# Kernel optimization log

Measured on AMD Instinct MI355X. Metric: run time of the kernel, lower is better.

Reference implementation:

```python
import jax, jax.numpy as jnp
import numpy as np

HEAD_SIZE = 64


def setup_inputs() -> dict:
    key = jax.random.key(0)
    k1, k2, k3, k4 = jax.random.split(key, 4)
    B, T, E = 8, 2048, 1024
    x = jax.random.normal(k1, (B, T, E), dtype=jnp.float32)
    # nn.Linear(n_embd, head_size, bias=False) weights: [head_size, n_embd]
    s = 1.0 / np.sqrt(E)
    Wk = jax.random.uniform(k2, (HEAD_SIZE, E), jnp.float32, -s, s)
    Wq = jax.random.uniform(k3, (HEAD_SIZE, E), jnp.float32, -s, s)
    Wv = jax.random.uniform(k4, (HEAD_SIZE, E), jnp.float32, -s, s)
    return {"x": x, "Wk": Wk, "Wq": Wq, "Wv": Wv}


def reference(x, Wk, Wq, Wv):
    # x: [B, T, E]; W*: [D, E] with D = head_size
    B, T, E = x.shape
    k = jnp.einsum("bte,de->btd", x, Wk)  # [B,T,D]
    q = jnp.einsum("bte,de->btd", x, Wq)
    v = jnp.einsum("bte,de->btd", x, Wv)
    scale = k.shape[-1] ** -0.5
    wei = jnp.einsum("btd,bsd->bts", q, k) * scale  # [B,T,T]
    causal = jnp.tril(jnp.ones((T, T), dtype=bool))
    wei = jnp.where(causal, wei, -jnp.inf)
    wei = jax.nn.softmax(wei, axis=-1)
    # dropout p=0.0 (eval): identity
    return jnp.einsum("bts,bsd->btd", wei, v)
```

## Files before the change

### kernel.cpp

```cpp
#include <hip/hip_runtime.h>
#include <hip/hip_bf16.h>


typedef __bf16 bf16x8 __attribute__((ext_vector_type(8)));
typedef float  f32x4  __attribute__((ext_vector_type(4)));

#define T_SEQ 2048
#define E_DIM 1024
#define D_HEAD 64
#define M_TOT 16384
#define NSPLIT 4
#define SC_LOG2E 0.18033688011112042f

__device__ __forceinline__ unsigned short f2b(float f) {
  union { float f; unsigned int u; } cv; cv.f = f;
  unsigned int u = cv.u;
  u += 0x7FFFu + ((u >> 16) & 1u);
  return (unsigned short)(u >> 16);
}

__device__ __forceinline__ unsigned int f2b2(float a, float b) {
#if __has_builtin(__builtin_amdgcn_cvt_pk_bf16_f32)
  typedef __bf16 bf16x2_t __attribute__((ext_vector_type(2)));
  union { bf16x2_t v; unsigned int u; } cv;
  cv.v = __builtin_amdgcn_cvt_pk_bf16_f32(a, b);
  return cv.u;
#else
  return (unsigned int)f2b(a) | ((unsigned int)f2b(b) << 16);
#endif
}

__global__ __launch_bounds__(256) void wcvt_kernel(
    const float* __restrict__ Wk, const float* __restrict__ Wq,
    const float* __restrict__ Wv, unsigned short* __restrict__ WbF)
{
  int i = blockIdx.x * 256 + threadIdx.x;
  int n = i >> 8, c4 = i & 255;
  const float* src = (n < 64) ? Wq + n * E_DIM
                   : (n < 128) ? Wk + (n - 64) * E_DIM
                               : Wv + (n - 128) * E_DIM;
  float4 v = *(const float4*)(src + c4 * 4);
  int k = c4 * 4, kb = k >> 5, kk = k & 31;
  *(uint2*)(WbF + (size_t)(kb * 192 + n) * 32 + kk) =
      make_uint2(f2b2(v.x, v.y), f2b2(v.z, v.w));
}

__global__ __launch_bounds__(256, 4) void proj_kernel(
    const float* __restrict__ x, const unsigned short* __restrict__ WbF,
    unsigned short* __restrict__ qws, unsigned short* __restrict__ kfws,
    unsigned short* __restrict__ vfws)
{
  __shared__ __align__(16) unsigned short x_lds[16 * 1024];

  const int tid = threadIdx.x, wv = tid >> 6, lane = tid & 63;
  const int c = lane & 15, quad = lane >> 4;
  const int m0 = blockIdx.x * 16;
  const int b = m0 >> 11, tloc = m0 & 2047;

  for (int j = 0; j < 16; ++j) {
    float4 v = *(const float4*)(x + (size_t)(m0 + j) * E_DIM + tid * 4);
    int chunk = tid >> 1, half = tid & 1;
    int phys = chunk ^ (j & 7);
    *(uint2*)&x_lds[j * 1024 + phys * 8 + half * 4] =
        make_uint2(f2b2(v.x, v.y), f2b2(v.z, v.w));
  }
  __syncthreads();

  f32x4 acc[3];
  for (int j = 0; j < 3; ++j)
    for (int r = 0; r < 4; ++r) acc[j][r] = 0.0f;

  const unsigned short* bbase[3];
  for (int j = 0; j < 3; ++j)
    bbase[j] = WbF + (size_t)((wv * 3 + j) * 16 + c) * 32 + quad * 8;

  bf16x8 bcur[3], bnxt[3];
  for (int j = 0; j < 3; ++j) bcur[j] = *(const bf16x8*)(bbase[j]);

  for (int kb = 0; kb < 32; ++kb) {
    if (kb < 31)
      for (int j = 0; j < 3; ++j)
        bnxt[j] = *(const bf16x8*)(bbase[j] + (size_t)(kb + 1) * 6144);
    bf16x8 a = *(const bf16x8*)&x_lds[c * 1024 + (((kb * 4 + quad) ^ (c & 7)) << 3)];
    for (int j = 0; j < 3; ++j)
      acc[j] = __builtin_amdgcn_mfma_f32_16x16x32_bf16(a, bcur[j], acc[j], 0, 0, 0);
    for (int j = 0; j < 3; ++j) bcur[j] = bnxt[j];
  }

  const int rloc = tloc + quad * 4;
  for (int j = 0; j < 3; ++j) {
    const int nt = wv * 3 + j;
    if (nt < 4) {
      int d = nt * 16 + c;
      for (int r = 0; r < 4; ++r)
        qws[(size_t)(m0 + quad * 4 + r) * D_HEAD + d] = f2b(acc[j][r] * SC_LOG2E);
    } else if (nt < 8) {
      int d = (nt - 4) * 16 + c;
      size_t base = ((size_t)(b * 2 + (d >> 5)) * T_SEQ + rloc) * 32 + (d & 31);
      for (int r = 0; r < 4; ++r)
        kfws[base + (size_t)r * 32] = f2b(acc[j][r]);
    } else {
      int d = (nt - 8) * 16 + c;
      size_t base = ((size_t)(b * 64 + (rloc >> 5)) * 64 + d) * 32 + (rloc & 31);
      *(ushort4*)&vfws[base] =
          make_ushort4(f2b(acc[j][0]), f2b(acc[j][1]), f2b(acc[j][2]), f2b(acc[j][3]));
    }
  }
}

__global__ __launch_bounds__(256, 4) void attn_kernel(
    const unsigned short* __restrict__ qws, const unsigned short* __restrict__ kfws,
    const unsigned short* __restrict__ vfws,
    unsigned short* __restrict__ opart, float* __restrict__ lpart)
{
  __shared__ __align__(16) unsigned short p_lds[64 * 64];

  const int tid = threadIdx.x, wv = tid >> 6, lane = tid & 63;
  const int c = lane & 15, quad = lane >> 4;
  const int qt = blockIdx.x, b = blockIdx.y, sg = blockIdx.z;
  const int t0 = qt * 64;
  const size_t qkb = (size_t)b * T_SEQ * D_HEAD;
  const int niter = (qt >= sg) ? ((qt - sg) >> 2) + 1 : 0;
  const int rloc = wv * 16 + quad * 4;
  const size_t prow = ((size_t)sg * 8 + b) * T_SEQ;

  if (niter == 0) {
    for (int nt = 0; nt < 4; ++nt)
      for (int r = 0; r < 4; ++r)
        opart[(prow + t0 + rloc + r) * D_HEAD + nt * 16 + c] = 0;
    if (c == 0)
      for (int r = 0; r < 4; ++r) lpart[prow + t0 + rloc + r] = 0.0f;
    return;
  }

  const int mrow = wv * 16 + c;
  const bf16x8 qf0 = *(const bf16x8*)(qws + qkb + (size_t)(t0 + mrow) * D_HEAD + quad * 8);
  const bf16x8 qf1 = *(const bf16x8*)(qws + qkb + (size_t)(t0 + mrow) * D_HEAD + 32 + quad * 8);

  bf16x8 ones;
  { union { unsigned short s[8]; bf16x8 v; } o;
    for (int i = 0; i < 8; ++i) o.s[i] = 0x3F80;
    ones = o.v; }

  f32x4 acc_o[4], acc_l;
  for (int r = 0; r < 4; ++r) acc_l[r] = 0.0f;
  for (int nt = 0; nt < 4; ++nt)
    for (int r = 0; r < 4; ++r) acc_o[nt][r] = 0.0f;

  const unsigned short* Kb = kfws + (size_t)b * 2 * T_SEQ * 32;
  const unsigned short* Vb = vfws + (size_t)b * 64 * D_HEAD * 32;
  const bool mydiag = (sg == (qt & 3));

  for (int it = 0; it < niter; ++it) {
    const int s0 = (sg + 4 * it) * 64;

    bf16x8 kf[8];
    for (int nt = 0; nt < 4; ++nt)
      for (int kb = 0; kb < 2; ++kb)
        kf[nt * 2 + kb] = *(const bf16x8*)(Kb + ((size_t)kb * T_SEQ + s0 + nt * 16 + c) * 32 + quad * 8);

    bf16x8 vf[8];
    for (int ks = 0; ks < 2; ++ks) {
      int sb = (s0 >> 5) + ks;
      for (int nt = 0; nt < 4; ++nt)
        vf[ks * 4 + nt] = *(const bf16x8*)(Vb + ((size_t)sb * 64 + nt * 16 + c) * 32 + quad * 8);
    }

    f32x4 accs[4];
    for (int nt = 0; nt < 4; ++nt)
      for (int r = 0; r < 4; ++r) accs[nt][r] = 0.0f;
    for (int nt = 0; nt < 4; ++nt) {
      accs[nt] = __builtin_amdgcn_mfma_f32_16x16x32_bf16(qf0, kf[nt * 2], accs[nt], 0, 0, 0);
      accs[nt] = __builtin_amdgcn_mfma_f32_16x16x32_bf16(qf1, kf[nt * 2 + 1], accs[nt], 0, 0, 0);
    }
    if (mydiag && it == niter - 1) {
      for (int nt = 0; nt < 4; ++nt) {
        int scol = s0 + nt * 16 + c;
        for (int r = 0; r < 4; ++r)
          if (scol > t0 + rloc + r) accs[nt][r] = -__builtin_inff();
      }
    }

    for (int nt = 0; nt < 4; ++nt)
      for (int r = 0; r < 4; ++r)
        accs[nt][r] = __builtin_exp2f(accs[nt][r]);

    for (int nt = 0; nt < 4; ++nt)
      for (int r = 0; r < 4; ++r) {
        int rr = rloc + r;
        p_lds[rr * 64 + (((nt * 2 + (c >> 3)) ^ (rr & 7)) << 3) + (c & 7)] = f2b(accs[nt][r]);
      }

    for (int ks = 0; ks < 2; ++ks) {
      int kg = ks * 4 + quad;
      bf16x8 pf = *(const bf16x8*)&p_lds[mrow * 64 + ((kg ^ (mrow & 7)) << 3)];
      acc_l = __builtin_amdgcn_mfma_f32_16x16x32_bf16(pf, ones, acc_l, 0, 0, 0);
      for (int nt = 0; nt < 4; ++nt)
        acc_o[nt] = __builtin_amdgcn_mfma_f32_16x16x32_bf16(pf, vf[ks * 4 + nt], acc_o[nt], 0, 0, 0);
    }
  }

  for (int nt = 0; nt < 4; ++nt)
    for (int r = 0; r < 4; ++r)
      opart[(prow + t0 + rloc + r) * D_HEAD + nt * 16 + c] = f2b(acc_o[nt][r]);
  if (c == 0)
    for (int r = 0; r < 4; ++r) lpart[prow + t0 + rloc + r] = acc_l[r];
}

__global__ __launch_bounds__(256) void merge_kernel(
    const unsigned short* __restrict__ opart, const float* __restrict__ lpart,
    float* __restrict__ out)
{
  int gid = blockIdx.x * 256 + threadIdx.x;
  int gr = gid >> 4, d4 = (gid & 15) * 4;
  float L = 0.0f;
  for (int i = 0; i < NSPLIT; ++i) L += lpart[(size_t)i * M_TOT + gr];
  float inv = 1.0f / L;
  float4 o = make_float4(0.f, 0.f, 0.f, 0.f);
  for (int i = 0; i < NSPLIT; ++i) {
    ushort4 u = *(const ushort4*)(opart + (size_t)i * M_TOT * D_HEAD + (size_t)gr * D_HEAD + d4);
    union { unsigned int u; float f; } cx, cy, cz, cw;
    cx.u = (unsigned int)u.x << 16; cy.u = (unsigned int)u.y << 16;
    cz.u = (unsigned int)u.z << 16; cw.u = (unsigned int)u.w << 16;
    o.x += cx.f; o.y += cy.f; o.z += cz.f; o.w += cw.f;
  }
  o.x *= inv; o.y *= inv; o.z *= inv; o.w *= inv;
  *(float4*)(out + (size_t)gr * D_HEAD + d4) = o;
}

extern "C" void kernel_launch(void* const* d_in, const int* in_sizes, int n_in,
                              void* d_out, int out_size, void* d_ws, size_t ws_size,
                              hipStream_t stream) {
  const float* x  = (const float*)d_in[0];
  const float* Wk = (const float*)d_in[1];
  const float* Wq = (const float*)d_in[2];
  const float* Wv = (const float*)d_in[3];
  float* out = (float*)d_out;

  unsigned short* qws   = (unsigned short*)d_ws;
  unsigned short* kfws  = qws + (size_t)M_TOT * D_HEAD;
  unsigned short* vfws  = kfws + (size_t)M_TOT * D_HEAD;
  unsigned short* WbF   = vfws + (size_t)M_TOT * D_HEAD;
  unsigned short* opart = WbF + 192 * E_DIM;
  float* lpart = (float*)(opart + (size_t)NSPLIT * M_TOT * D_HEAD);

  wcvt_kernel<<<192, 256, 0, stream>>>(Wk, Wq, Wv, WbF);
  proj_kernel<<<M_TOT / 16, 256, 0, stream>>>(x, WbF, qws, kfws, vfws);
  attn_kernel<<<dim3(T_SEQ / 64, 8, NSPLIT), 256, 0, stream>>>(qws, kfws, vfws, opart, lpart);
  merge_kernel<<<M_TOT * 16 / 256, 256, 0, stream>>>(opart, lpart, out);
}
```

Baseline: 153.9 us.

## Restructure projection into double-buffered LDS DMA pipeline and prefetch K in attention

The projection kernel now processes 64 rows per 1024-thread block. It stages fp32 x tiles and bf16 weight tiles into double-buffered LDS using global_load_lds DMA with XOR swizzles, and converts x to bf16 at fragment load time. This lets the 64 rows share each weight tile from LDS instead of every 16-row block streaming all weights through registers. The attention kernel also prefetches the next iteration's K fragments after the QK MFMAs to hide load latency. The cost is more LDS per block, larger blocks, and extra registers for the prefetched K.

```diff
diff --git a/kernel.cpp b/kernel.cpp
--- a/kernel.cpp
+++ b/kernel.cpp
@@ -30,9 +30,15 @@
 #endif
 }
 
+__device__ __forceinline__ void dma16(const void* g, void* l) {
+  __builtin_amdgcn_global_load_lds(
+      (const __attribute__((address_space(1))) void*)g,
+      (__attribute__((address_space(3))) void*)l, 16, 0, 0);
+}
+
 __global__ __launch_bounds__(256) void wcvt_kernel(
     const float* __restrict__ Wk, const float* __restrict__ Wq,
-    const float* __restrict__ Wv, unsigned short* __restrict__ WbF)
+    const float* __restrict__ Wv, unsigned short* __restrict__ Wb)
 {
   int i = blockIdx.x * 256 + threadIdx.x;
   int n = i >> 8, c4 = i & 255;
@@ -40,68 +46,85 @@
                    : (n < 128) ? Wk + (n - 64) * E_DIM
                                : Wv + (n - 128) * E_DIM;
   float4 v = *(const float4*)(src + c4 * 4);
-  int k = c4 * 4, kb = k >> 5, kk = k & 31;
-  *(uint2*)(WbF + (size_t)(kb * 192 + n) * 32 + kk) =
-      make_uint2(f2b2(v.x, v.y), f2b2(v.z, v.w));
-}
-
-__global__ __launch_bounds__(256, 4) void proj_kernel(
-    const float* __restrict__ x, const unsigned short* __restrict__ WbF,
+  *(uint2*)(Wb + (size_t)n * E_DIM + c4 * 4) = make_uint2(f2b2(v.x, v.y), f2b2(v.z, v.w));
+}
+
+__global__ __launch_bounds__(1024, 4) void proj_kernel(
+    const float* __restrict__ x, const unsigned short* __restrict__ Wb,
     unsigned short* __restrict__ qws, unsigned short* __restrict__ kfws,
     unsigned short* __restrict__ vfws)
 {
-  __shared__ __align__(16) unsigned short x_lds[16 * 1024];
+  __shared__ __align__(16) float x_lds[2][64 * 64];
+  __shared__ __align__(16) unsigned short w_lds[2][192 * 64];
 
   const int tid = threadIdx.x, wv = tid >> 6, lane = tid & 63;
   const int c = lane & 15, quad = lane >> 4;
-  const int m0 = blockIdx.x * 16;
+  const int mi = wv & 3, ng = wv >> 2;
+  const int m0 = blockIdx.x * 64;
   const int b = m0 >> 11, tloc = m0 & 2047;
 
-  for (int j = 0; j < 16; ++j) {
-    float4 v = *(const float4*)(x + (size_t)(m0 + j) * E_DIM + tid * 4);
-    int chunk = tid >> 1, half = tid & 1;
-    int phys = chunk ^ (j & 7);
-    *(uint2*)&x_lds[j * 1024 + phys * 8 + half * 4] =
-        make_uint2(f2b2(v.x, v.y), f2b2(v.z, v.w));
-  }
-  __syncthreads();
+  const int xr = tid >> 4, xp = tid & 15;
+  const float* xsrc = x + (size_t)(m0 + xr) * E_DIM + ((xp ^ (xr & 15)) << 2);
+  const int wro = lane >> 3, wp = lane & 7;
+
+  auto stage = [&](int s, int buf) {
+    const int k0 = s * 64;
+    dma16(xsrc + k0, &x_lds[buf][wv * 256]);
+    {
+      int r = wv * 8 + wro;
+      dma16(Wb + (size_t)r * E_DIM + k0 + ((wp ^ (r & 7)) << 3), &w_lds[buf][wv * 512]);
+    }
+    if (wv < 8) {
+      int r = (wv + 16) * 8 + wro;
+      dma16(Wb + (size_t)r * E_DIM + k0 + ((wp ^ (r & 7)) << 3), &w_lds[buf][(wv + 16) * 512]);
+    }
+  };
 
   f32x4 acc[3];
   for (int j = 0; j < 3; ++j)
     for (int r = 0; r < 4; ++r) acc[j][r] = 0.0f;
 
-  const unsigned short* bbase[3];
-  for (int j = 0; j < 3; ++j)
-    bbase[j] = WbF + (size_t)((wv * 3 + j) * 16 + c) * 32 + quad * 8;
-
-  bf16x8 bcur[3], bnxt[3];
-  for (int j = 0; j < 3; ++j) bcur[j] = *(const bf16x8*)(bbase[j]);
-
-  for (int kb = 0; kb < 32; ++kb) {
-    if (kb < 31)
-      for (int j = 0; j < 3; ++j)
-        bnxt[j] = *(const bf16x8*)(bbase[j] + (size_t)(kb + 1) * 6144);
-    bf16x8 a = *(const bf16x8*)&x_lds[c * 1024 + (((kb * 4 + quad) ^ (c & 7)) << 3)];
-    for (int j = 0; j < 3; ++j)
-      acc[j] = __builtin_amdgcn_mfma_f32_16x16x32_bf16(a, bcur[j], acc[j], 0, 0, 0);
-    for (int j = 0; j < 3; ++j) bcur[j] = bnxt[j];
-  }
-
-  const int rloc = tloc + quad * 4;
+  stage(0, 0);
+  __syncthreads();
+
+  const int arow = mi * 16 + c;
+  for (int s = 0; s < 16; ++s) {
+    const int cur = s & 1;
+    if (s < 15) stage(s + 1, cur ^ 1);
+    const float* xb = x_lds[cur];
+    const unsigned short* wb = w_lds[cur];
+    for (int kb = 0; kb < 2; ++kb) {
+      const int g0 = kb * 8 + quad * 2;
+      f32x4 r1 = *(const f32x4*)&xb[arow * 64 + ((g0 ^ (arow & 15)) << 2)];
+      f32x4 r2 = *(const f32x4*)&xb[arow * 64 + (((g0 + 1) ^ (arow & 15)) << 2)];
+      union { unsigned int u[4]; bf16x8 v; } A;
+      A.u[0] = f2b2(r1[0], r1[1]); A.u[1] = f2b2(r1[2], r1[3]);
+      A.u[2] = f2b2(r2[0], r2[1]); A.u[3] = f2b2(r2[2], r2[3]);
+      for (int j = 0; j < 3; ++j) {
+        const int n = (ng * 3 + j) * 16 + c;
+        bf16x8 bb = *(const bf16x8*)&wb[n * 64 + (((kb * 4 + quad) ^ (n & 7)) << 3)];
+        acc[j] = __builtin_amdgcn_mfma_f32_16x16x32_bf16(A.v, bb, acc[j], 0, 0, 0);
+      }
+    }
+    if (s < 15) __syncthreads();
+  }
+
+  const int rg = m0 + mi * 16 + quad * 4;
+  const int sl = tloc + mi * 16 + quad * 4;
   for (int j = 0; j < 3; ++j) {
-    const int nt = wv * 3 + j;
+    const int nt = ng * 3 + j;
     if (nt < 4) {
       int d = nt * 16 + c;
       for (int r = 0; r < 4; ++r)
-        qws[(size_t)(m0 + quad * 4 + r) * D_HEAD + d] = f2b(acc[j][r] * SC_LOG2E);
+        qws[(size_t)(rg + r) * D_HEAD + d] = f2b(acc[j][r] * SC_LOG2E);
     } else if (nt < 8) {
       int d = (nt - 4) * 16 + c;
-      size_t base = ((size_t)(b * 2 + (d >> 5)) * T_SEQ + rloc) * 32 + (d & 31);
+      size_t base = ((size_t)(b * 2 + (d >> 5)) * T_SEQ + sl) * 32 + (d & 31);
       for (int r = 0; r < 4; ++r)
         kfws[base + (size_t)r * 32] = f2b(acc[j][r]);
     } else {
       int d = (nt - 8) * 16 + c;
-      size_t base = ((size_t)(b * 64 + (rloc >> 5)) * 64 + d) * 32 + (rloc & 31);
+      size_t base = ((size_t)(b * 64 + (sl >> 5)) * 64 + d) * 32 + (sl & 31);
       *(ushort4*)&vfws[base] =
           make_ushort4(f2b(acc[j][0]), f2b(acc[j][1]), f2b(acc[j][2]), f2b(acc[j][3]));
     }
@@ -151,13 +174,16 @@
   const unsigned short* Vb = vfws + (size_t)b * 64 * D_HEAD * 32;
   const bool mydiag = (sg == (qt & 3));
 
+  bf16x8 kf[8];
+  {
+    const int s0 = sg * 64;
+    for (int nt = 0; nt < 4; ++nt)
+      for (int kb = 0; kb < 2; ++kb)
+        kf[nt * 2 + kb] = *(const bf16x8*)(Kb + ((size_t)kb * T_SEQ + s0 + nt * 16 + c) * 32 + quad * 8);
+  }
+
   for (int it = 0; it < niter; ++it) {
     const int s0 = (sg + 4 * it) * 64;
-
-    bf16x8 kf[8];
-    for (int nt = 0; nt < 4; ++nt)
-      for (int kb = 0; kb < 2; ++kb)
-        kf[nt * 2 + kb] = *(const bf16x8*)(Kb + ((size_t)kb * T_SEQ + s0 + nt * 16 + c) * 32 + quad * 8);
 
     bf16x8 vf[8];
     for (int ks = 0; ks < 2; ++ks) {
@@ -173,6 +199,14 @@
       accs[nt] = __builtin_amdgcn_mfma_f32_16x16x32_bf16(qf0, kf[nt * 2], accs[nt], 0, 0, 0);
       accs[nt] = __builtin_amdgcn_mfma_f32_16x16x32_bf16(qf1, kf[nt * 2 + 1], accs[nt], 0, 0, 0);
     }
+
+    if (it + 1 < niter) {
+      const int s0n = s0 + 256;
+      for (int nt = 0; nt < 4; ++nt)
+        for (int kb = 0; kb < 2; ++kb)
+          kf[nt * 2 + kb] = *(const bf16x8*)(Kb + ((size_t)kb * T_SEQ + s0n + nt * 16 + c) * 32 + quad * 8);
+    }
+
     if (mydiag && it == niter - 1) {
       for (int nt = 0; nt < 4; ++nt) {
         int scol = s0 + nt * 16 + c;
@@ -240,12 +274,12 @@
   unsigned short* qws   = (unsigned short*)d_ws;
   unsigned short* kfws  = qws + (size_t)M_TOT * D_HEAD;
   unsigned short* vfws  = kfws + (size_t)M_TOT * D_HEAD;
-  unsigned short* WbF   = vfws + (size_t)M_TOT * D_HEAD;
-  unsigned short* opart = WbF + 192 * E_DIM;
+  unsigned short* Wb    = vfws + (size_t)M_TOT * D_HEAD;
+  unsigned short* opart = Wb + 192 * E_DIM;
   float* lpart = (float*)(opart + (size_t)NSPLIT * M_TOT * D_HEAD);
 
-  wcvt_kernel<<<192, 256, 0, stream>>>(Wk, Wq, Wv, WbF);
-  proj_kernel<<<M_TOT / 16, 256, 0, stream>>>(x, WbF, qws, kfws, vfws);
+  wcvt_kernel<<<192, 256, 0, stream>>>(Wk, Wq, Wv, Wb);
+  proj_kernel<<<M_TOT / 64, 1024, 0, stream>>>(x, Wb, qws, kfws, vfws);
   attn_kernel<<<dim3(T_SEQ / 64, 8, NSPLIT), 256, 0, stream>>>(qws, kfws, vfws, opart, lpart);
   merge_kernel<<<M_TOT * 16 / 256, 256, 0, stream>>>(opart, lpart, out);
 }
```

Result: slower. 170.1 us (+10.5%).
